# Kernel optimization log

Measured on AMD Instinct MI355X. Metric: run time of the kernel, lower is better.

Reference implementation:

```python
import jax, jax.numpy as jnp
import numpy as np

B, S, H = 4, 512, 256

def setup_inputs() -> dict:
    key = jax.random.key(0)
    k1, k2, k3, k4 = jax.random.split(key, 4)
    scale = 1.0 / np.sqrt(H)
    return {
        "h": jax.random.normal(k1, (B, S, H), dtype=jnp.float32),
        "W_t": jax.random.normal(k2, (H, H), dtype=jnp.float32) * scale,
        "W_t_prime": jax.random.normal(k3, (H, H), dtype=jnp.float32) * scale,
        "b_h": jnp.zeros((H,), dtype=jnp.float32),
        "W_a": jax.random.normal(k4, (H,), dtype=jnp.float32) * scale,
        "b_a": jnp.zeros((), dtype=jnp.float32),
    }

def reference(h, W_t, W_t_prime, b_h, W_a, b_a):
    # Project once per timestep, then broadcast-add over the (t, t') pair grid.
    ht = jnp.einsum("bsh,hk->bsk", h, W_t)          # W_t applied to h^t
    htp = jnp.einsum("bsh,hk->bsk", h, W_t_prime)   # W_{t'} applied to h^{t'}
    # transformed: (B, S_t, S_t', H)
    transformed = ht[:, :, None, :] + htp[:, None, :, :] + b_h
    tanh_out = jnp.tanh(transformed)
    scores = jnp.einsum("bsth,h->bst", tanh_out, W_a) + b_a  # (B, S, S)
    scores = jax.nn.sigmoid(scores)
    attention_weights = jax.nn.softmax(scores, axis=2)
    output = jnp.einsum("bst,bth->bsh", attention_weights, h)
    return output, attention_weights
```

## Files before the change

### kernel.cpp

```cpp
#include <hip/hip_runtime.h>

#define Bn 4
#define Sn 512
#define Hn 256

#define CC   2.8853900817779268f
#define L2E  1.4426950408889634f

typedef __attribute__((ext_vector_type(4))) float f32x4;
typedef __attribute__((ext_vector_type(8))) short short8;

__device__ __forceinline__ unsigned short bf16rn(float f) {
    unsigned int u = __float_as_uint(f);
    u += 0x7fffu + ((u >> 16) & 1u);
    return (unsigned short)(u >> 16);
}
__device__ __forceinline__ float bf16tof(unsigned short b) {
    return __uint_as_float(((unsigned int)b) << 16);
}

__global__ __launch_bounds__(256) void splitA_kernel(
    const float* __restrict__ h, const float* __restrict__ Wa,
    const float* __restrict__ ba,
    unsigned short* __restrict__ h1, unsigned short* __restrict__ h2,
    float* __restrict__ wa2, float* __restrict__ cst)
{
    __shared__ float red4[4];
    const int tid = threadIdx.x;
    const int base = (blockIdx.x * 256 + tid) * 8;

    float4 v0 = *(const float4*)&h[base];
    float4 v1 = *(const float4*)&h[base + 4];
    float f[8] = {v0.x, v0.y, v0.z, v0.w, v1.x, v1.y, v1.z, v1.w};
    unsigned short b1[8], b2[8];
#pragma unroll
    for (int i = 0; i < 8; i++) {
        b1[i] = bf16rn(f[i]);
        b2[i] = bf16rn(f[i] - bf16tof(b1[i]));
    }
    uint4 u1, u2;
    u1.x = (unsigned)b1[0] | ((unsigned)b1[1] << 16);
    u1.y = (unsigned)b1[2] | ((unsigned)b1[3] << 16);
    u1.z = (unsigned)b1[4] | ((unsigned)b1[5] << 16);
    u1.w = (unsigned)b1[6] | ((unsigned)b1[7] << 16);
    u2.x = (unsigned)b2[0] | ((unsigned)b2[1] << 16);
    u2.y = (unsigned)b2[2] | ((unsigned)b2[3] << 16);
    u2.z = (unsigned)b2[4] | ((unsigned)b2[5] << 16);
    u2.w = (unsigned)b2[6] | ((unsigned)b2[7] << 16);
    *(uint4*)&h1[base] = u1;
    *(uint4*)&h2[base] = u2;

    if (blockIdx.x == 0) {
        float w = Wa[tid];
#pragma unroll
        for (int off = 32; off >= 1; off >>= 1) w += __shfl_xor(w, off, 64);
        if ((tid & 63) == 0) red4[tid >> 6] = w;
        __syncthreads();
        wa2[tid] = -2.0f * Wa[tid];
        if (tid == 0)
            cst[0] = -L2E * ((red4[0] + red4[1] + red4[2] + red4[3]) + ba[0]);
    }
}

__global__ __launch_bounds__(256) void splitB_kernel(
    const float* __restrict__ Wt, const float* __restrict__ Wp,
    unsigned short* __restrict__ wtp)
{
    __shared__ float tile[64 * 68];
    const int tid = threadIdx.x;
    const int mat = blockIdx.x >> 4;
    const int t4  = blockIdx.x & 15;
    const int k0  = (t4 >> 2) * 64, n0 = (t4 & 3) * 64;
    const float* __restrict__ W = mat ? Wp : Wt;

#pragma unroll
    for (int i = 0; i < 4; i++) {
        const int idx = tid + 256 * i;
        const int kr = idx >> 4, nq = idx & 15;
        *(float4*)&tile[kr * 68 + nq * 4] =
            *(const float4*)&W[(k0 + kr) * Hn + n0 + nq * 4];
    }
    __syncthreads();

    unsigned short* p1 = wtp + mat * 2 * 65536;
    unsigned short* p2 = p1 + 65536;
#pragma unroll
    for (int i = 0; i < 8; i++) {
        const int idx = tid + 256 * i;
        const int n = idx >> 5, kp = idx & 31;
        const float f0 = tile[(2 * kp) * 68 + n];
        const float f1 = tile[(2 * kp + 1) * 68 + n];
        const unsigned short a0 = bf16rn(f0), a1 = bf16rn(f1);
        const unsigned short c0 = bf16rn(f0 - bf16tof(a0));
        const unsigned short c1 = bf16rn(f1 - bf16tof(a1));
        const int dw = ((n0 + n) * 256 + k0) / 2 + kp;
        ((unsigned int*)p1)[dw] = (unsigned)a0 | ((unsigned)a1 << 16);
        ((unsigned int*)p2)[dw] = (unsigned)c0 | ((unsigned)c1 << 16);
    }
}

__global__ __launch_bounds__(256) void gemm_kernel(
    const unsigned short* __restrict__ h1, const unsigned short* __restrict__ h2,
    const unsigned short* __restrict__ wtp, const float* __restrict__ bh,
    float* __restrict__ Egt, float* __restrict__ Egp4)
{
    __shared__ char lds[20480];

    const int tid = threadIdx.x;
    const int mb = blockIdx.x >> 3;
    const int nb = blockIdx.x & 7;
    const int m0 = mb * 64;
    const bool isT = (nb < 4);
    const int n0l = isT ? nb * 64 : (nb - 4) * 64;
    const unsigned short* pB1 = wtp + (isT ? 0 : 2 * 65536);
    const unsigned short* pB2 = pB1 + 65536;

    const int w    = tid >> 6;
    const int lane = tid & 63;
    const int quad = lane >> 4;
    const int l15  = lane & 15;

    f32x4 acc[4];
#pragma unroll
    for (int i = 0; i < 4; i++) acc[i] = (f32x4){0.f, 0.f, 0.f, 0.f};

    const int ssel = tid >> 7;
    const int spl  = (tid >> 6) & 1;
    const int srow = (tid & 63) >> 2;
    const int sseg = tid & 3;
    const unsigned short* gsrc =
        (ssel == 0) ? (spl ? h2 : h1) : (spl ? pB2 : pB1);
    const int growbase = (ssel == 0) ? m0 : n0l;
    char* ldsdst = lds + (ssel * 2 + spl) * 5120;

    for (int ks = 0; ks < 256; ks += 32) {
        __syncthreads();
#pragma unroll
        for (int i = 0; i < 4; i++) {
            const int row = srow + i * 16;
            uint4 v = *(const uint4*)&gsrc[(growbase + row) * 256 + ks + sseg * 8];
            *(uint4*)(ldsdst + row * 80 + sseg * 16) = v;
        }
        __syncthreads();

        const char* Ab = lds;
        const char* Bb = lds + 10240;
        const short8 b1 = *(const short8*)(Bb + (w * 16 + l15) * 80 + quad * 16);
        const short8 b2 = *(const short8*)(Bb + 5120 + (w * 16 + l15) * 80 + quad * 16);
#pragma unroll
        for (int mt = 0; mt < 4; mt++) {
            const short8 a1 = *(const short8*)(Ab + (mt * 16 + l15) * 80 + quad * 16);
            const short8 a2 = *(const short8*)(Ab + 5120 + (mt * 16 + l15) * 80 + quad * 16);
            acc[mt] = __builtin_amdgcn_mfma_f32_16x16x32_bf16(a1, b1, acc[mt], 0, 0, 0);
            acc[mt] = __builtin_amdgcn_mfma_f32_16x16x32_bf16(a1, b2, acc[mt], 0, 0, 0);
            acc[mt] = __builtin_amdgcn_mfma_f32_16x16x32_bf16(a2, b1, acc[mt], 0, 0, 0);
        }
    }

    __syncthreads();
    float* ct = (float*)lds;
#pragma unroll
    for (int mt = 0; mt < 4; mt++)
#pragma unroll
        for (int r = 0; r < 4; r++)
            ct[(mt * 16 + quad * 4 + r) * 68 + w * 16 + l15] = acc[mt][r];
    __syncthreads();

    const int b  = m0 >> 9;
    const int s0 = m0 & 511;
    if (isT) {
        const int n0g = nb * 64;
#pragma unroll
        for (int i = 0; i < 4; i++) {
            const int item = tid + i * 256;
            const int mr = item >> 4, nq = item & 15;
            const float4 c  = *(const float4*)&ct[mr * 68 + nq * 4];
            const float4 bv = *(const float4*)&bh[n0g + nq * 4];
            float4 o;
            o.x = __builtin_amdgcn_exp2f((c.x + bv.x) * CC);
            o.y = __builtin_amdgcn_exp2f((c.y + bv.y) * CC);
            o.z = __builtin_amdgcn_exp2f((c.z + bv.z) * CC);
            o.w = __builtin_amdgcn_exp2f((c.w + bv.w) * CC);
            *(float4*)&Egt[(m0 + mr) * Hn + n0g + nq * 4] = o;
        }
    } else {
        const int kq0 = (nb - 4) * 16;
#pragma unroll
        for (int i = 0; i < 4; i++) {
            const int item = tid + i * 256;
            const int mr = item & 63, nq = item >> 6;
            const float4 c = *(const float4*)&ct[mr * 68 + nq * 4];
            float4 o;
            o.x = __builtin_amdgcn_exp2f(c.x * CC);
            o.y = __builtin_amdgcn_exp2f(c.y * CC);
            o.z = __builtin_amdgcn_exp2f(c.z * CC);
            o.w = __builtin_amdgcn_exp2f(c.w * CC);
            *(float4*)&Egp4[b * 131072 + (kq0 + nq) * 2048 + (s0 + mr) * 4] = o;
        }
    }
}

__global__ __launch_bounds__(512) void score_kernel(
    const float* __restrict__ Egt,  const float* __restrict__ Egp4,
    const float* __restrict__ wa2,  const float* __restrict__ cst,
    float* __restrict__ out_attn)
{
    __shared__ float egt4[4 * Hn];
    __shared__ float wal[Hn];
    __shared__ float red[4][8];

    const int tid = threadIdx.x;
    const int b   = blockIdx.x & 3;
    const int t0  = (blockIdx.x >> 2) << 2;

    egt4[tid]       = Egt[(b * Sn + t0) * Hn + tid];
    egt4[512 + tid] = Egt[(b * Sn + t0) * Hn + 512 + tid];
    if (tid < 256) wal[tid] = wa2[tid];
    __syncthreads();

    const float4* __restrict__ ep = (const float4*)(Egp4 + b * (Hn * Sn));
    const int tp = tid;

    float acc[4] = {0.f, 0.f, 0.f, 0.f};

    float4 cur = ep[tp];
#pragma unroll 2
    for (int k4 = 0; k4 < 64; k4++) {
        float4 nxt = cur;
        if (k4 < 63) nxt = ep[(k4 + 1) * Sn + tp];
        const float4 w4 = *(const float4*)&wal[k4 * 4];
#pragma unroll
        for (int r = 0; r < 4; r++) {
            const float4 eg = *(const float4*)&egt4[r * Hn + k4 * 4];
            const float d1 = fmaf(cur.x, eg.x, 1.0f);
            const float d2 = fmaf(cur.y, eg.y, 1.0f);
            const float d3 = fmaf(cur.z, eg.z, 1.0f);
            const float d4 = fmaf(cur.w, eg.w, 1.0f);
            const float p12 = d1 * d2, p34 = d3 * d4;
            const float n12 = fmaf(w4.x, d2, w4.y * d1);
            const float n34 = fmaf(w4.z, d4, w4.w * d3);
            const float num = fmaf(n12, p34, n34 * p12);
            acc[r] = fmaf(num, __builtin_amdgcn_rcpf(p12 * p34), acc[r]);
        }
        cur = nxt;
    }

    const float k0 = cst[0];
    float ex[4];
#pragma unroll
    for (int r = 0; r < 4; r++) {
        const float e1  = __builtin_amdgcn_exp2f(fmaf(-L2E, acc[r], k0));
        const float sig = __builtin_amdgcn_rcpf(1.0f + e1);
        ex[r] = __builtin_amdgcn_exp2f(L2E * sig);
    }

    const int lane = tid & 63, wid = tid >> 6;
#pragma unroll
    for (int r = 0; r < 4; r++) {
        float v = ex[r];
#pragma unroll
        for (int off = 32; off >= 1; off >>= 1) v += __shfl_xor(v, off, 64);
        if (lane == 0) red[r][wid] = v;
    }
    __syncthreads();

#pragma unroll
    for (int r = 0; r < 4; r++) {
        const float tot = red[r][0] + red[r][1] + red[r][2] + red[r][3] +
                          red[r][4] + red[r][5] + red[r][6] + red[r][7];
        out_attn[(b * Sn + t0 + r) * Sn + tp] = ex[r] * __builtin_amdgcn_rcpf(tot);
    }
}

__global__ __launch_bounds__(512) void out_kernel(
    const float* __restrict__ hsrc, const float* __restrict__ attn,
    float* __restrict__ out)
{
    __shared__ float4 part[4 * 8 * 64];

    const int tid = threadIdx.x;
    const int b   = blockIdx.x & 3;
    const int t0  = (blockIdx.x >> 2) << 3;
    const int c4  = tid & 63;
    const int q   = __builtin_amdgcn_readfirstlane(tid >> 6);

    const float* __restrict__ ar = attn + (b * Sn + t0) * Sn + q * 64;
    const float* __restrict__ hb = hsrc + (b * Sn + q * 64) * Hn + c4 * 4;

    float4 a[8];
#pragma unroll
    for (int r = 0; r < 8; r++) a[r] = (float4){0.f, 0.f, 0.f, 0.f};

#pragma unroll 2
    for (int j4 = 0; j4 < 16; j4++) {
        float4 wv[8];
#pragma unroll
        for (int r = 0; r < 8; r++)
            wv[r] = *(const float4*)&ar[r * Sn + j4 * 4];
#pragma unroll
        for (int i = 0; i < 4; i++) {
            const float4 hv = *(const float4*)&hb[(j4 * 4 + i) * Hn];
#pragma unroll
            for (int r = 0; r < 8; r++) {
                const float wr = ((const float*)&wv[r])[i];
                a[r].x = fmaf(wr, hv.x, a[r].x);
                a[r].y = fmaf(wr, hv.y, a[r].y);
                a[r].z = fmaf(wr, hv.z, a[r].z);
                a[r].w = fmaf(wr, hv.w, a[r].w);
            }
        }
    }

    if (q < 4) {
#pragma unroll
        for (int r = 0; r < 8; r++) part[(q * 8 + r) * 64 + c4] = a[r];
    }
    __syncthreads();
    if (q >= 4) {
#pragma unroll
        for (int r = 0; r < 8; r++) {
            float4 p = part[((q - 4) * 8 + r) * 64 + c4];
            p.x += a[r].x; p.y += a[r].y; p.z += a[r].z; p.w += a[r].w;
            part[((q - 4) * 8 + r) * 64 + c4] = p;
        }
    }
    __syncthreads();

    const int col = tid & 255;
    const int rs  = tid >> 8;
    const float* pf = (const float*)part;
#pragma unroll
    for (int rr = 0; rr < 4; rr++) {
        const int r = rs * 4 + rr;
        float s = 0.f;
#pragma unroll
        for (int qq = 0; qq < 4; qq++)
            s += pf[((qq * 8 + r) * 64 + (col >> 2)) * 4 + (col & 3)];
        out[(b * Sn + t0 + r) * Hn + col] = s;
    }
}

extern "C" void kernel_launch(void* const* d_in, const int* in_sizes, int n_in,
                              void* d_out, int out_size, void* d_ws, size_t ws_size,
                              hipStream_t stream) {
    const float* h   = (const float*)d_in[0];
    const float* Wt  = (const float*)d_in[1];
    const float* Wtp = (const float*)d_in[2];
    const float* bh  = (const float*)d_in[3];
    const float* Wa  = (const float*)d_in[4];
    const float* ba  = (const float*)d_in[5];

    float* out      = (float*)d_out;
    float* out_attn = out + Bn * Sn * Hn;

    float* ws   = (float*)d_ws;
    float* Egt  = ws;
    float* Egp4 = ws + 524288;
    float* wa2  = ws + 1048576;
    float* cst  = ws + 1048832;
    unsigned short* h1  = (unsigned short*)(ws + 1048840);
    unsigned short* h2  = h1 + 2048 * 256;
    unsigned short* wtp = h2 + 2048 * 256;

    splitA_kernel<<<dim3(256), dim3(256), 0, stream>>>(h, Wa, ba, h1, h2, wa2, cst);
    splitB_kernel<<<dim3(32), dim3(256), 0, stream>>>(Wt, Wtp, wtp);
    gemm_kernel<<<dim3(256), dim3(256), 0, stream>>>(h1, h2, wtp, bh, Egt, Egp4);
    score_kernel<<<dim3(Bn * (Sn / 4)), dim3(512), 0, stream>>>(Egt, Egp4, wa2, cst, out_attn);
    out_kernel<<<dim3(Bn * (Sn / 8)), dim3(512), 0, stream>>>(h, out_attn, out);
}
```

Baseline: 124.1 us.

## Fuse prep kernels and merge score with output matmul via LDS

Measured after the change: 125.1 us. Within noise of the previous version (+0.8%).

```diff
diff --git a/kernel.cpp b/kernel.cpp
--- a/kernel.cpp
+++ b/kernel.cpp
@@ -19,83 +19,83 @@
     return __uint_as_float(((unsigned int)b) << 16);
 }
 
-__global__ __launch_bounds__(256) void splitA_kernel(
-    const float* __restrict__ h, const float* __restrict__ Wa,
+__global__ __launch_bounds__(256) void prep_kernel(
+    const float* __restrict__ h,  const float* __restrict__ Wt,
+    const float* __restrict__ Wp, const float* __restrict__ Wa,
     const float* __restrict__ ba,
     unsigned short* __restrict__ h1, unsigned short* __restrict__ h2,
+    unsigned short* __restrict__ wtp,
     float* __restrict__ wa2, float* __restrict__ cst)
 {
+    __shared__ float tile[64 * 68];
     __shared__ float red4[4];
     const int tid = threadIdx.x;
-    const int base = (blockIdx.x * 256 + tid) * 8;
-
-    float4 v0 = *(const float4*)&h[base];
-    float4 v1 = *(const float4*)&h[base + 4];
-    float f[8] = {v0.x, v0.y, v0.z, v0.w, v1.x, v1.y, v1.z, v1.w};
-    unsigned short b1[8], b2[8];
-#pragma unroll
-    for (int i = 0; i < 8; i++) {
-        b1[i] = bf16rn(f[i]);
-        b2[i] = bf16rn(f[i] - bf16tof(b1[i]));
-    }
-    uint4 u1, u2;
-    u1.x = (unsigned)b1[0] | ((unsigned)b1[1] << 16);
-    u1.y = (unsigned)b1[2] | ((unsigned)b1[3] << 16);
-    u1.z = (unsigned)b1[4] | ((unsigned)b1[5] << 16);
-    u1.w = (unsigned)b1[6] | ((unsigned)b1[7] << 16);
-    u2.x = (unsigned)b2[0] | ((unsigned)b2[1] << 16);
-    u2.y = (unsigned)b2[2] | ((unsigned)b2[3] << 16);
-    u2.z = (unsigned)b2[4] | ((unsigned)b2[5] << 16);
-    u2.w = (unsigned)b2[6] | ((unsigned)b2[7] << 16);
-    *(uint4*)&h1[base] = u1;
-    *(uint4*)&h2[base] = u2;
-
-    if (blockIdx.x == 0) {
-        float w = Wa[tid];
-#pragma unroll
-        for (int off = 32; off >= 1; off >>= 1) w += __shfl_xor(w, off, 64);
-        if ((tid & 63) == 0) red4[tid >> 6] = w;
+    const int bid = blockIdx.x;
+
+    if (bid < 256) {
+        const int base = (bid * 256 + tid) * 8;
+        float4 v0 = *(const float4*)&h[base];
+        float4 v1 = *(const float4*)&h[base + 4];
+        float f[8] = {v0.x, v0.y, v0.z, v0.w, v1.x, v1.y, v1.z, v1.w};
+        unsigned short b1[8], b2[8];
+#pragma unroll
+        for (int i = 0; i < 8; i++) {
+            b1[i] = bf16rn(f[i]);
+            b2[i] = bf16rn(f[i] - bf16tof(b1[i]));
+        }
+        uint4 u1, u2;
+        u1.x = (unsigned)b1[0] | ((unsigned)b1[1] << 16);
+        u1.y = (unsigned)b1[2] | ((unsigned)b1[3] << 16);
+        u1.z = (unsigned)b1[4] | ((unsigned)b1[5] << 16);
+        u1.w = (unsigned)b1[6] | ((unsigned)b1[7] << 16);
+        u2.x = (unsigned)b2[0] | ((unsigned)b2[1] << 16);
+        u2.y = (unsigned)b2[2] | ((unsigned)b2[3] << 16);
+        u2.z = (unsigned)b2[4] | ((unsigned)b2[5] << 16);
+        u2.w = (unsigned)b2[6] | ((unsigned)b2[7] << 16);
+        *(uint4*)&h1[base] = u1;
+        *(uint4*)&h2[base] = u2;
+
+        if (bid == 0) {
+            float w = Wa[tid];
+#pragma unroll
+            for (int off = 32; off >= 1; off >>= 1) w += __shfl_xor(w, off, 64);
+            if ((tid & 63) == 0) red4[tid >> 6] = w;
+            __syncthreads();
+            wa2[tid] = -2.0f * Wa[tid];
+            if (tid == 0)
+                cst[0] = -L2E * ((red4[0] + red4[1] + red4[2] + red4[3]) + ba[0]);
+        }
+    } else {
+        const int sb  = bid - 256;
+        const int mat = sb >> 4;
+        const int t4  = sb & 15;
+        const int k0  = (t4 >> 2) * 64, n0 = (t4 & 3) * 64;
+        const float* __restrict__ W = mat ? Wp : Wt;
+
+#pragma unroll
+        for (int i = 0; i < 4; i++) {
+            const int idx = tid + 256 * i;
+            const int kr = idx >> 4, nq = idx & 15;
+            *(float4*)&tile[kr * 68 + nq * 4] =
+                *(const float4*)&W[(k0 + kr) * Hn + n0 + nq * 4];
+        }
         __syncthreads();
-        wa2[tid] = -2.0f * Wa[tid];
-        if (tid == 0)
-            cst[0] = -L2E * ((red4[0] + red4[1] + red4[2] + red4[3]) + ba[0]);
-    }
-}
-
-__global__ __launch_bounds__(256) void splitB_kernel(
-    const float* __restrict__ Wt, const float* __restrict__ Wp,
-    unsigned short* __restrict__ wtp)
-{
-    __shared__ float tile[64 * 68];
-    const int tid = threadIdx.x;
-    const int mat = blockIdx.x >> 4;
-    const int t4  = blockIdx.x & 15;
-    const int k0  = (t4 >> 2) * 64, n0 = (t4 & 3) * 64;
-    const float* __restrict__ W = mat ? Wp : Wt;
-
-#pragma unroll
-    for (int i = 0; i < 4; i++) {
-        const int idx = tid + 256 * i;
-        const int kr = idx >> 4, nq = idx & 15;
-        *(float4*)&tile[kr * 68 + nq * 4] =
-            *(const float4*)&W[(k0 + kr) * Hn + n0 + nq * 4];
-    }
-    __syncthreads();
-
-    unsigned short* p1 = wtp + mat * 2 * 65536;
-    unsigned short* p2 = p1 + 65536;
-#pragma unroll
-    for (int i = 0; i < 8; i++) {
-        const int idx = tid + 256 * i;
-        const int n = idx >> 5, kp = idx & 31;
-        const float f0 = tile[(2 * kp) * 68 + n];
-        const float f1 = tile[(2 * kp + 1) * 68 + n];
-        const unsigned short a0 = bf16rn(f0), a1 = bf16rn(f1);
-        const unsigned short c0 = bf16rn(f0 - bf16tof(a0));
-        const unsigned short c1 = bf16rn(f1 - bf16tof(a1));
-        const int dw = ((n0 + n) * 256 + k0) / 2 + kp;
-        ((unsigned int*)p1)[dw] = (unsigned)a0 | ((unsigned)a1 << 16);
-        ((unsigned int*)p2)[dw] = (unsigned)c0 | ((unsigned)c1 << 16);
+
+        unsigned short* p1 = wtp + mat * 2 * 65536;
+        unsigned short* p2 = p1 + 65536;
+#pragma unroll
+        for (int i = 0; i < 8; i++) {
+            const int idx = tid + 256 * i;
+            const int n = idx >> 5, kp = idx & 31;
+            const float f0 = tile[(2 * kp) * 68 + n];
+            const float f1 = tile[(2 * kp + 1) * 68 + n];
+            const unsigned short a0 = bf16rn(f0), a1 = bf16rn(f1);
+            const unsigned short c0 = bf16rn(f0 - bf16tof(a0));
+            const unsigned short c1 = bf16rn(f1 - bf16tof(a1));
+            const int dw = ((n0 + n) * 256 + k0) / 2 + kp;
+            ((unsigned int*)p1)[dw] = (unsigned)a0 | ((unsigned)a1 << 16);
+            ((unsigned int*)p2)[dw] = (unsigned)c0 | ((unsigned)c1 << 16);
+        }
     }
 }
 
@@ -200,38 +200,42 @@
     }
 }
 
-__global__ __launch_bounds__(512) void score_kernel(
-    const float* __restrict__ Egt,  const float* __restrict__ Egp4,
-    const float* __restrict__ wa2,  const float* __restrict__ cst,
-    float* __restrict__ out_attn)
+__global__ __launch_bounds__(512) void attn_kernel(
+    const float* __restrict__ hsrc, const float* __restrict__ Egt,
+    const float* __restrict__ Egp4, const float* __restrict__ wa2,
+    const float* __restrict__ cst,
+    float* __restrict__ out, float* __restrict__ out_attn)
 {
-    __shared__ float egt4[4 * Hn];
-    __shared__ float wal[Hn];
-    __shared__ float red[4][8];
+    __shared__ char smem[49152];
+    float*  egt8   = (float*)smem;
+    float*  attn_l = (float*)smem;
+    float*  wal    = (float*)(smem + 16384);
+    float*  red    = (float*)(smem + 17408);
+    float4* part   = (float4*)(smem + 16384);
 
     const int tid = threadIdx.x;
     const int b   = blockIdx.x & 3;
-    const int t0  = (blockIdx.x >> 2) << 2;
-
-    egt4[tid]       = Egt[(b * Sn + t0) * Hn + tid];
-    egt4[512 + tid] = Egt[(b * Sn + t0) * Hn + 512 + tid];
+    const int t0  = (blockIdx.x >> 2) << 3;
+
+    for (int i = tid; i < 8 * Hn; i += 512)
+        egt8[i] = Egt[(b * Sn + t0) * Hn + i];
     if (tid < 256) wal[tid] = wa2[tid];
     __syncthreads();
 
     const float4* __restrict__ ep = (const float4*)(Egp4 + b * (Hn * Sn));
-    const int tp = tid;
-
-    float acc[4] = {0.f, 0.f, 0.f, 0.f};
-
-    float4 cur = ep[tp];
-#pragma unroll 2
+
+    float acc[8];
+#pragma unroll
+    for (int r = 0; r < 8; r++) acc[r] = 0.f;
+
+    float4 cur = ep[tid];
+    float4 nxt = ep[Sn + tid];
     for (int k4 = 0; k4 < 64; k4++) {
-        float4 nxt = cur;
-        if (k4 < 63) nxt = ep[(k4 + 1) * Sn + tp];
+        const float4 nn = ep[((k4 + 2) & 63) * Sn + tid];
         const float4 w4 = *(const float4*)&wal[k4 * 4];
 #pragma unroll
-        for (int r = 0; r < 4; r++) {
-            const float4 eg = *(const float4*)&egt4[r * Hn + k4 * 4];
+        for (int r = 0; r < 8; r++) {
+            const float4 eg = *(const float4*)&egt8[r * Hn + k4 * 4];
             const float d1 = fmaf(cur.x, eg.x, 1.0f);
             const float d2 = fmaf(cur.y, eg.y, 1.0f);
             const float d3 = fmaf(cur.z, eg.z, 1.0f);
@@ -242,13 +246,13 @@
             const float num = fmaf(n12, p34, n34 * p12);
             acc[r] = fmaf(num, __builtin_amdgcn_rcpf(p12 * p34), acc[r]);
         }
-        cur = nxt;
+        cur = nxt; nxt = nn;
     }
 
     const float k0 = cst[0];
-    float ex[4];
-#pragma unroll
-    for (int r = 0; r < 4; r++) {
+    float ex[8];
+#pragma unroll
+    for (int r = 0; r < 8; r++) {
         const float e1  = __builtin_amdgcn_exp2f(fmaf(-L2E, acc[r], k0));
         const float sig = __builtin_amdgcn_rcpf(1.0f + e1);
         ex[r] = __builtin_amdgcn_exp2f(L2E * sig);
@@ -256,35 +260,28 @@
 
     const int lane = tid & 63, wid = tid >> 6;
 #pragma unroll
-    for (int r = 0; r < 4; r++) {
+    for (int r = 0; r < 8; r++) {
         float v = ex[r];
 #pragma unroll
         for (int off = 32; off >= 1; off >>= 1) v += __shfl_xor(v, off, 64);
-        if (lane == 0) red[r][wid] = v;
-    }
-    __syncthreads();
-
-#pragma unroll
-    for (int r = 0; r < 4; r++) {
-        const float tot = red[r][0] + red[r][1] + red[r][2] + red[r][3] +
-                          red[r][4] + red[r][5] + red[r][6] + red[r][7];
-        out_attn[(b * Sn + t0 + r) * Sn + tp] = ex[r] * __builtin_amdgcn_rcpf(tot);
-    }
-}
-
-__global__ __launch_bounds__(512) void out_kernel(
-    const float* __restrict__ hsrc, const float* __restrict__ attn,
-    float* __restrict__ out)
-{
-    __shared__ float4 part[4 * 8 * 64];
-
-    const int tid = threadIdx.x;
-    const int b   = blockIdx.x & 3;
-    const int t0  = (blockIdx.x >> 2) << 3;
-    const int c4  = tid & 63;
-    const int q   = __builtin_amdgcn_readfirstlane(tid >> 6);
-
-    const float* __restrict__ ar = attn + (b * Sn + t0) * Sn + q * 64;
+        if (lane == 0) red[r * 8 + wid] = v;
+    }
+    __syncthreads();
+
+#pragma unroll
+    for (int r = 0; r < 8; r++) {
+        float tot = 0.f;
+#pragma unroll
+        for (int i = 0; i < 8; i++) tot += red[r * 8 + i];
+        const float a = ex[r] * __builtin_amdgcn_rcpf(tot);
+        attn_l[r * Sn + tid] = a;
+        out_attn[(b * Sn + t0 + r) * Sn + tid] = a;
+    }
+    __syncthreads();
+
+    const int c4 = tid & 63;
+    const int q  = __builtin_amdgcn_readfirstlane(tid >> 6);
+
     const float* __restrict__ hb = hsrc + (b * Sn + q * 64) * Hn + c4 * 4;
 
     float4 a[8];
@@ -296,7 +293,7 @@
         float4 wv[8];
 #pragma unroll
         for (int r = 0; r < 8; r++)
-            wv[r] = *(const float4*)&ar[r * Sn + j4 * 4];
+            wv[r] = *(const float4*)&attn_l[r * Sn + q * 64 + j4 * 4];
 #pragma unroll
         for (int i = 0; i < 4; i++) {
             const float4 hv = *(const float4*)&hb[(j4 * 4 + i) * Hn];
@@ -310,6 +307,7 @@
             }
         }
     }
+    __syncthreads();
 
     if (q < 4) {
 #pragma unroll
@@ -362,9 +360,9 @@
     unsigned short* h2  = h1 + 2048 * 256;
     unsigned short* wtp = h2 + 2048 * 256;
 
-    splitA_kernel<<<dim3(256), dim3(256), 0, stream>>>(h, Wa, ba, h1, h2, wa2, cst);
-    splitB_kernel<<<dim3(32), dim3(256), 0, stream>>>(Wt, Wtp, wtp);
+    prep_kernel<<<dim3(288), dim3(256), 0, stream>>>(
+        h, Wt, Wtp, Wa, ba, h1, h2, wtp, wa2, cst);
     gemm_kernel<<<dim3(256), dim3(256), 0, stream>>>(h1, h2, wtp, bh, Egt, Egp4);
-    score_kernel<<<dim3(Bn * (Sn / 4)), dim3(512), 0, stream>>>(Egt, Egp4, wa2, cst, out_attn);
-    out_kernel<<<dim3(Bn * (Sn / 8)), dim3(512), 0, stream>>>(h, out_attn, out);
-}
+    attn_kernel<<<dim3(Bn * (Sn / 8)), dim3(512), 0, stream>>>(
+        h, Egt, Egp4, wa2, cst, out, out_attn);
+}
```
